# Kernel tuning notes

Hardware: AMD Instinct MI355X
Metric: run time of the kernel (lower is better)

Reference implementation:

```python
import jax, jax.numpy as jnp
import numpy as np

N, E = 50000, 800000
IN_C, HID, OUT_C, HEADS = 256, 32, 16, 8
NEG_SLOPE = 0.2


def gat_conv(x, edge_index, W, att_src, att_dst, bias, heads, out_c, concat):
    """PyG-style GATConv (inference, dropout off, add_self_loops=True).

    x: [N, F_in], edge_index: [2, E] with row0=src(j), row1=dst(i).
    W: [F_in, heads*out_c], att_src/att_dst: [heads, out_c], bias: [heads*out_c] or [out_c].
    """
    n = x.shape[0]
    loops = jnp.arange(n, dtype=edge_index.dtype)
    src = jnp.concatenate([edge_index[0], loops])
    dst = jnp.concatenate([edge_index[1], loops])

    xl = (x @ W).reshape(n, heads, out_c)              # [N, H, C]
    a_src = jnp.einsum('nhc,hc->nh', xl, att_src)      # [N, H]
    a_dst = jnp.einsum('nhc,hc->nh', xl, att_dst)

    e = a_src[src] + a_dst[dst]                        # [E', H]
    e = jnp.where(e >= 0, e, NEG_SLOPE * e)            # leaky_relu
    e_max = jax.ops.segment_max(e, dst, num_segments=n)
    e_exp = jnp.exp(e - e_max[dst])
    denom = jax.ops.segment_sum(e_exp, dst, num_segments=n)
    alpha = e_exp / (denom[dst] + 1e-16)               # segment softmax over in-edges of dst

    msg = alpha[:, :, None] * xl[src]                  # [E', H, C]
    out = jax.ops.segment_sum(msg, dst, num_segments=n)  # [N, H, C]
    if concat:
        out = out.reshape(n, heads * out_c)
    else:
        out = out.mean(axis=1)
    return out + bias


def setup_inputs() -> dict:
    key = jax.random.key(0)
    ks = jax.random.split(key, 10)
    s_in = 1.0 / np.sqrt(IN_C)
    s_h = 1.0 / np.sqrt(HEADS * HID)
    x = jax.random.normal(ks[0], (N, IN_C), dtype=jnp.float32)
    edge_index = jax.random.randint(ks[1], (2, E), 0, N, dtype=jnp.int64)
    return {
        'x': x,
        'edge_index': edge_index,
        'W1': jax.random.normal(ks[2], (IN_C, HEADS * HID), dtype=jnp.float32) * s_in,
        'att_src1': jax.random.normal(ks[3], (HEADS, HID), dtype=jnp.float32) * s_h,
        'att_dst1': jax.random.normal(ks[4], (HEADS, HID), dtype=jnp.float32) * s_h,
        'b1': jnp.zeros((HEADS * HID,), dtype=jnp.float32),
        'W2': jax.random.normal(ks[5], (HEADS * HID, OUT_C), dtype=jnp.float32) * s_h,
        'att_src2': jax.random.normal(ks[6], (1, OUT_C), dtype=jnp.float32) * 0.1,
        'att_dst2': jax.random.normal(ks[7], (1, OUT_C), dtype=jnp.float32) * 0.1,
        'b2': jnp.zeros((OUT_C,), dtype=jnp.float32),
    }


def reference(x, edge_index, W1, att_src1, att_dst1, b1, W2, att_src2, att_dst2, b2):
    h = gat_conv(x, edge_index, W1, att_src1, att_dst1, b1, HEADS, HID, concat=True)
    h = jax.nn.relu(h)
    # F.dropout(training=False) is identity at inference
    out = gat_conv(h, edge_index, W2, att_src2, att_dst2, b2, 1, OUT_C, concat=False)
    return jax.nn.log_softmax(out, axis=1)
```

## Files before the change

kernel.cpp:

```cpp
#include <hip/hip_runtime.h>

#define IN_C 256
#define H1 8
#define C1 32
#define F1 256
#define OC 16
#define NEG 0.2f

typedef short short8 __attribute__((ext_vector_type(8)));
typedef unsigned short ushort8 __attribute__((ext_vector_type(8)));
typedef float floatx4 __attribute__((ext_vector_type(4)));

__device__ __forceinline__ unsigned short f2bf(float f) {
    unsigned u = __builtin_bit_cast(unsigned, f);
    u = (u + 0x7fffu + ((u >> 16) & 1u)) >> 16;
    return (unsigned short)u;
}
__device__ __forceinline__ float bf2f(unsigned short h) {
    unsigned u = ((unsigned)h) << 16;
    return __builtin_bit_cast(float, u);
}

__global__ __launch_bounds__(256) void k_cvt_x(const float* __restrict__ x,
                                               unsigned short* __restrict__ xb, int n4)
{
    int idx = blockIdx.x * 256 + threadIdx.x;
    if (idx >= n4) return;
    float4 v = ((const float4*)x)[idx];
    ushort4 o;
    o.x = f2bf(v.x); o.y = f2bf(v.y); o.z = f2bf(v.z); o.w = f2bf(v.w);
    ((ushort4*)xb)[idx] = o;
}

__global__ __launch_bounds__(256) void k_wcvt(const float* __restrict__ W1,
                                              const float* __restrict__ W2,
                                              unsigned short* __restrict__ w1t,
                                              unsigned short* __restrict__ w2t)
{
    int idx = blockIdx.x * 256 + threadIdx.x;
    if (idx < 65536) {
        int n = idx >> 8, k = idx & 255;
        w1t[n * 256 + k] = f2bf(W1[k * 256 + n]);
    } else if (idx < 65536 + 4096) {
        int r = idx - 65536;
        int n = r >> 8, k = r & 255;
        w2t[n * 256 + k] = f2bf(W2[k * 16 + n]);
    }
}

__global__ __launch_bounds__(256) void k_gemm1(const unsigned short* __restrict__ A,
                                               const unsigned short* __restrict__ Bt,
                                               unsigned short* __restrict__ Cb, int M)
{
    __shared__ short As[128][40];
    __shared__ short Bs[128][40];
    const int tid  = threadIdx.x;
    const int lane = tid & 63;
    const int w    = tid >> 6;
    const int bm   = blockIdx.x * 128;
    const int bn   = blockIdx.y * 128;
    const int wm   = (w >> 1) * 64;
    const int wn   = (w & 1) * 64;
    const int srow = tid >> 1;
    const int soff = (tid & 1) * 16;
    floatx4 acc[4][4] = {};
    for (int k0 = 0; k0 < 256; k0 += 32) {
        __syncthreads();
        {
            int gr = bm + srow;
            ushort8 v0 = {0,0,0,0,0,0,0,0}, v1 = {0,0,0,0,0,0,0,0};
            if (gr < M) {
                const ushort8* p = (const ushort8*)(A + (size_t)gr * 256 + k0 + soff);
                v0 = p[0]; v1 = p[1];
            }
            *(ushort8*)&As[srow][soff]     = v0;
            *(ushort8*)&As[srow][soff + 8] = v1;
        }
        {
            const ushort8* p = (const ushort8*)(Bt + (size_t)(bn + srow) * 256 + k0 + soff);
            *(ushort8*)&Bs[srow][soff]     = p[0];
            *(ushort8*)&Bs[srow][soff + 8] = p[1];
        }
        __syncthreads();
        short8 af[4], bf[4];
        const int q8 = (lane >> 4) * 8;
        const int l15 = lane & 15;
#pragma unroll
        for (int i = 0; i < 4; ++i) af[i] = *(const short8*)&As[wm + i * 16 + l15][q8];
#pragma unroll
        for (int j = 0; j < 4; ++j) bf[j] = *(const short8*)&Bs[wn + j * 16 + l15][q8];
#pragma unroll
        for (int i = 0; i < 4; ++i)
#pragma unroll
            for (int j = 0; j < 4; ++j)
                acc[i][j] = __builtin_amdgcn_mfma_f32_16x16x32_bf16(af[i], bf[j], acc[i][j], 0, 0, 0);
    }
    const int l15 = lane & 15;
    const int rq  = (lane >> 4) * 4;
#pragma unroll
    for (int i = 0; i < 4; ++i) {
#pragma unroll
        for (int reg = 0; reg < 4; ++reg) {
            int gr = bm + wm + i * 16 + rq + reg;
            if (gr < M) {
#pragma unroll
                for (int j = 0; j < 4; ++j)
                    Cb[(size_t)gr * 256 + bn + wn + j * 16 + l15] = f2bf(acc[i][j][reg]);
            }
        }
    }
}

__global__ __launch_bounds__(256) void k_att1(const unsigned short* __restrict__ xl,
                                              const float* __restrict__ att_s,
                                              const float* __restrict__ att_d,
                                              float* __restrict__ asrc,
                                              float* __restrict__ adst, int N)
{
    int idx = blockIdx.x * 256 + threadIdx.x;
    if (idx >= N * H1) return;
    int i = idx >> 3, h = idx & 7;
    const ushort4* xr = (const ushort4*)(xl + (size_t)i * F1 + h * C1);
    const float* s = att_s + h * C1;
    const float* d = att_d + h * C1;
    float s1 = 0.f, s2 = 0.f;
#pragma unroll
    for (int c4 = 0; c4 < 8; ++c4) {
        ushort4 v = xr[c4];
        float f0 = bf2f(v.x), f1 = bf2f(v.y), f2 = bf2f(v.z), f3 = bf2f(v.w);
        int c = c4 * 4;
        s1 += f0 * s[c] + f1 * s[c+1] + f2 * s[c+2] + f3 * s[c+3];
        s2 += f0 * d[c] + f1 * d[c+1] + f2 * d[c+2] + f3 * d[c+3];
    }
    asrc[idx] = s1; adst[idx] = s2;
}

__global__ __launch_bounds__(256) void k_hist(const int* __restrict__ ei,
                                              int* __restrict__ cnt, int E)
{
    int e = blockIdx.x * 256 + threadIdx.x;
    if (e < E) atomicAdd(&cnt[ei[E + e]], 1);
}

__global__ __launch_bounds__(256) void k_scan_a(const int* __restrict__ cnt,
                                                int* __restrict__ rp,
                                                int* __restrict__ bsum, int N)
{
    __shared__ int ws4[4];
    int t = threadIdx.x, lane = t & 63, wid = t >> 6;
    int i = blockIdx.x * 256 + t;
    int v = (i < N) ? cnt[i] : 0;
    int incl = v;
#pragma unroll
    for (int off = 1; off < 64; off <<= 1) {
        int tv = __shfl_up(incl, off, 64);
        if (lane >= off) incl += tv;
    }
    if (lane == 63) ws4[wid] = incl;
    __syncthreads();
    int add = 0;
    for (int w = 0; w < wid; ++w) add += ws4[w];
    incl += add;
    if (i < N) rp[i + 1] = incl;
    if (t == 255) bsum[blockIdx.x] = incl;
}

__global__ __launch_bounds__(256) void k_scan_b(const int* __restrict__ bsum,
                                                int* __restrict__ boff, int NB)
{
    __shared__ int ws4[4];
    int t = threadIdx.x, lane = t & 63, wid = t >> 6;
    int i0 = t * 4;
    int v[4];
#pragma unroll
    for (int k = 0; k < 4; ++k) { int i = i0 + k; v[k] = (i < NB) ? bsum[i] : 0; }
    int s = v[0] + v[1] + v[2] + v[3];
    int incl = s;
#pragma unroll
    for (int off = 1; off < 64; off <<= 1) {
        int tv = __shfl_up(incl, off, 64);
        if (lane >= off) incl += tv;
    }
    if (lane == 63) ws4[wid] = incl;
    __syncthreads();
    int wpre = 0;
    for (int w = 0; w < wid; ++w) wpre += ws4[w];
    int run = wpre + incl - s;
#pragma unroll
    for (int k = 0; k < 4; ++k) {
        int i = i0 + k;
        if (i < NB) boff[i] = run;
        run += v[k];
    }
}

__global__ __launch_bounds__(256) void k_scan_c(int* __restrict__ rp,
                                                const int* __restrict__ boff, int N)
{
    int i = blockIdx.x * 256 + threadIdx.x;
    if (i < N) rp[i + 1] += boff[blockIdx.x];
    if (i == 0) rp[0] = 0;
}

__global__ __launch_bounds__(256) void k_scatter(const int* __restrict__ ei,
                                                 int* __restrict__ cur,
                                                 int* __restrict__ ssrc, int E)
{
    int e = blockIdx.x * 256 + threadIdx.x;
    if (e >= E) return;
    int s = ei[e];
    int d = ei[E + e];
    int pos = atomicAdd(&cur[d], 1);
    ssrc[pos] = s;
}

__global__ __launch_bounds__(256) void k_gather1(const int* __restrict__ rp,
                                                 const int* __restrict__ ssrc,
                                                 const unsigned short* __restrict__ xl,
                                                 const float* __restrict__ asrc,
                                                 const float* __restrict__ adst,
                                                 const float* __restrict__ bias,
                                                 unsigned short* __restrict__ hout, int N)
{
    int lane = threadIdx.x & 63;
    int node = blockIdx.x * 4 + (threadIdx.x >> 6);
    if (node >= N) return;
    int h  = lane >> 3;
    int cb = lane * 4;
    float ad = adst[(size_t)node * H1 + h];
    float e = asrc[(size_t)node * H1 + h] + ad;
    e = e >= 0.f ? e : NEG * e;
    float w = __expf(e);
    ushort4 xv = *(const ushort4*)(xl + (size_t)node * F1 + cb);
    float ax = w * bf2f(xv.x), ay = w * bf2f(xv.y), az = w * bf2f(xv.z), aw = w * bf2f(xv.w);
    float den = w;
    int jb = rp[node], je = rp[node + 1];
    int j = jb;
    for (; j + 4 <= je; j += 4) {
        int s0 = ssrc[j], s1 = ssrc[j+1], s2 = ssrc[j+2], s3 = ssrc[j+3];
        float e0 = asrc[(size_t)s0 * H1 + h] + ad;
        float e1 = asrc[(size_t)s1 * H1 + h] + ad;
        float e2 = asrc[(size_t)s2 * H1 + h] + ad;
        float e3 = asrc[(size_t)s3 * H1 + h] + ad;
        ushort4 r0 = *(const ushort4*)(xl + (size_t)s0 * F1 + cb);
        ushort4 r1 = *(const ushort4*)(xl + (size_t)s1 * F1 + cb);
        ushort4 r2 = *(const ushort4*)(xl + (size_t)s2 * F1 + cb);
        ushort4 r3 = *(const ushort4*)(xl + (size_t)s3 * F1 + cb);
        e0 = e0 >= 0.f ? e0 : NEG * e0;  float w0 = __expf(e0);
        e1 = e1 >= 0.f ? e1 : NEG * e1;  float w1 = __expf(e1);
        e2 = e2 >= 0.f ? e2 : NEG * e2;  float w2 = __expf(e2);
        e3 = e3 >= 0.f ? e3 : NEG * e3;  float w3 = __expf(e3);
        den += w0 + w1 + w2 + w3;
        ax += w0*bf2f(r0.x) + w1*bf2f(r1.x) + w2*bf2f(r2.x) + w3*bf2f(r3.x);
        ay += w0*bf2f(r0.y) + w1*bf2f(r1.y) + w2*bf2f(r2.y) + w3*bf2f(r3.y);
        az += w0*bf2f(r0.z) + w1*bf2f(r1.z) + w2*bf2f(r2.z) + w3*bf2f(r3.z);
        aw += w0*bf2f(r0.w) + w1*bf2f(r1.w) + w2*bf2f(r2.w) + w3*bf2f(r3.w);
    }
    for (; j < je; ++j) {
        int s = ssrc[j];
        float ev = asrc[(size_t)s * H1 + h] + ad;
        ev = ev >= 0.f ? ev : NEG * ev;
        float wv = __expf(ev);
        ushort4 sv = *(const ushort4*)(xl + (size_t)s * F1 + cb);
        ax += wv * bf2f(sv.x); ay += wv * bf2f(sv.y);
        az += wv * bf2f(sv.z); aw += wv * bf2f(sv.w);
        den += wv;
    }
    float inv = 1.f / (den + 1e-16f);
    float4 bv = *(const float4*)(bias + cb);
    ushort4 o;
    o.x = f2bf(fmaxf(ax * inv + bv.x, 0.f));
    o.y = f2bf(fmaxf(ay * inv + bv.y, 0.f));
    o.z = f2bf(fmaxf(az * inv + bv.z, 0.f));
    o.w = f2bf(fmaxf(aw * inv + bv.w, 0.f));
    *(ushort4*)(hout + (size_t)node * F1 + cb) = o;
}

__global__ __launch_bounds__(256) void k_gemm2(const unsigned short* __restrict__ Hm,
                                               const unsigned short* __restrict__ W2t,
                                               const float* __restrict__ as2,
                                               const float* __restrict__ ad2,
                                               unsigned short* __restrict__ xl2b,
                                               float* __restrict__ asrc,
                                               float* __restrict__ adst, int N)
{
    const int lane = threadIdx.x & 63;
    const int wid  = threadIdx.x >> 6;
    const int rowbase = blockIdx.x * 64 + wid * 16;
    const int col = lane & 15;
    const int q8  = (lane >> 4) * 8;
    const int m   = rowbase + col;
    const bool mv = m < N;
    const unsigned short* arow = Hm + (size_t)m * 256 + q8;
    const unsigned short* brow = W2t + (size_t)col * 256 + q8;
    floatx4 acc = {0.f, 0.f, 0.f, 0.f};
#pragma unroll
    for (int t = 0; t < 8; ++t) {
        short8 af = {0,0,0,0,0,0,0,0};
        if (mv) af = *(const short8*)(arow + t * 32);
        short8 bf = *(const short8*)(brow + t * 32);
        acc = __builtin_amdgcn_mfma_f32_16x16x32_bf16(af, bf, acc, 0, 0, 0);
    }
    float s_as = as2[col], s_ad = ad2[col];
    const int rq = (lane >> 4) * 4;
#pragma unroll
    for (int reg = 0; reg < 4; ++reg) {
        int row = rowbase + rq + reg;
        float v = acc[reg];
        float s1 = v * s_as, s2 = v * s_ad;
#pragma unroll
        for (int o = 1; o < 16; o <<= 1) { s1 += __shfl_xor(s1, o, 16); s2 += __shfl_xor(s2, o, 16); }
        if (row < N) {
            xl2b[(size_t)row * OC + col] = f2bf(v);
            if (col == 0) { asrc[row] = s1; adst[row] = s2; }
        }
    }
}

__global__ __launch_bounds__(256) void k_gather2(const int* __restrict__ rp,
                                                 const int* __restrict__ ssrc,
                                                 const unsigned short* __restrict__ xl2b,
                                                 const float* __restrict__ asrc,
                                                 const float* __restrict__ adst,
                                                 const float* __restrict__ bias,
                                                 float* __restrict__ out, int N)
{
    int sub  = threadIdx.x & 15;
    int node = blockIdx.x * 16 + (threadIdx.x >> 4);
    if (node >= N) return;
    float ad = adst[node];
    float e = asrc[node] + ad;
    e = e >= 0.f ? e : NEG * e;
    float w = __expf(e);
    float acc = w * bf2f(xl2b[(size_t)node * OC + sub]);
    float den = w;
    int jb = rp[node], je = rp[node + 1];
    int j = jb;
    for (; j + 4 <= je; j += 4) {
        int s0 = ssrc[j], s1i = ssrc[j+1], s2i = ssrc[j+2], s3i = ssrc[j+3];
        float e0 = asrc[s0] + ad, e1 = asrc[s1i] + ad, e2 = asrc[s2i] + ad, e3 = asrc[s3i] + ad;
        float v0 = bf2f(xl2b[(size_t)s0 * OC + sub]);
        float v1 = bf2f(xl2b[(size_t)s1i * OC + sub]);
        float v2 = bf2f(xl2b[(size_t)s2i * OC + sub]);
        float v3 = bf2f(xl2b[(size_t)s3i * OC + sub]);
        e0 = e0 >= 0.f ? e0 : NEG * e0;  float w0 = __expf(e0);
        e1 = e1 >= 0.f ? e1 : NEG * e1;  float w1 = __expf(e1);
        e2 = e2 >= 0.f ? e2 : NEG * e2;  float w2 = __expf(e2);
        e3 = e3 >= 0.f ? e3 : NEG * e3;  float w3 = __expf(e3);
        den += w0 + w1 + w2 + w3;
        acc += w0 * v0 + w1 * v1 + w2 * v2 + w3 * v3;
    }
    for (; j < je; ++j) {
        int s = ssrc[j];
        float ev = asrc[s] + ad;
        ev = ev >= 0.f ? ev : NEG * ev;
        float wv = __expf(ev);
        acc += wv * bf2f(xl2b[(size_t)s * OC + sub]);
        den += wv;
    }
    float v = acc / (den + 1e-16f) + bias[sub];
    float m = v;
#pragma unroll
    for (int o = 1; o < 16; o <<= 1) m = fmaxf(m, __shfl_xor(m, o, 16));
    float ex = __expf(v - m);
    float ss = ex;
#pragma unroll
    for (int o = 1; o < 16; o <<= 1) ss += __shfl_xor(ss, o, 16);
    out[(size_t)node * OC + sub] = v - m - logf(ss);
}

extern "C" void kernel_launch(void* const* d_in, const int* in_sizes, int n_in,
                              void* d_out, int out_size, void* d_ws, size_t ws_size,
                              hipStream_t stream)
{
    const float* x   = (const float*)d_in[0];
    const int*   ei  = (const int*)d_in[1];
    const float* W1  = (const float*)d_in[2];
    const float* as1 = (const float*)d_in[3];
    const float* ad1 = (const float*)d_in[4];
    const float* b1  = (const float*)d_in[5];
    const float* W2  = (const float*)d_in[6];
    const float* as2 = (const float*)d_in[7];
    const float* ad2 = (const float*)d_in[8];
    const float* b2  = (const float*)d_in[9];
    float* out = (float*)d_out;

    const int N = in_sizes[0] / IN_C;
    const int E = in_sizes[1] / 2;
    const int NB = (N + 255) / 256;

    char* base = (char*)d_ws;
    unsigned short* xb   = (unsigned short*)base;
    unsigned short* xl1b = xb + (size_t)N * F1;
    unsigned short* hb   = xl1b + (size_t)N * F1;
    unsigned short* w1t  = hb + (size_t)N * F1;
    unsigned short* w2t  = w1t + 256 * 256;
    unsigned short* xl2b = w2t + 16 * 256;
    float* asrc1 = (float*)(xl2b + (size_t)N * OC);
    float* adst1 = asrc1 + (size_t)N * H1;
    float* asrc2 = adst1 + (size_t)N * H1;
    float* adst2 = asrc2 + N;
    int*   rp    = (int*)(adst2 + N);
    int*   cnt   = rp + (N + 1);
    int*   cur   = cnt + N;
    int*   bsum  = cur + N;
    int*   boff  = bsum + 1024;
    int*   ssrc  = boff + 1024;

    hipMemsetAsync(cnt, 0, (size_t)N * sizeof(int), stream);
    k_hist<<<(E + 255) / 256, 256, 0, stream>>>(ei, cnt, E);
    k_scan_a<<<NB, 256, 0, stream>>>(cnt, rp, bsum, N);
    k_scan_b<<<1, 256, 0, stream>>>(bsum, boff, NB);
    k_scan_c<<<NB, 256, 0, stream>>>(rp, boff, N);
    hipMemcpyAsync(cur, rp, (size_t)N * sizeof(int), hipMemcpyDeviceToDevice, stream);
    k_scatter<<<(E + 255) / 256, 256, 0, stream>>>(ei, cur, ssrc, E);

    k_cvt_x<<<(N * 64 + 255) / 256, 256, 0, stream>>>(x, xb, N * 64);
    k_wcvt<<<(65536 + 4096) / 256, 256, 0, stream>>>(W1, W2, w1t, w2t);

    k_gemm1<<<dim3((N + 127) / 128, 2), 256, 0, stream>>>(xb, w1t, xl1b, N);
    k_att1<<<(N * H1 + 255) / 256, 256, 0, stream>>>(xl1b, as1, ad1, asrc1, adst1, N);
    k_gather1<<<(N + 3) / 4, 256, 0, stream>>>(rp, ssrc, xl1b, asrc1, adst1, b1, hb, N);

    k_gemm2<<<(N + 63) / 64, 256, 0, stream>>>(hb, w2t, as2, ad2, xl2b, asrc2, adst2, N);
    k_gather2<<<(N + 15) / 16, 256, 0, stream>>>(rp, ssrc, xl2b, asrc2, adst2, b2, out, N);
}
```

Measured before the change: 338.5 us.

## Split per-node edge aggregation across multiple waves/slots in both gather kernels

In the first-layer gather, each node's in-edge range is now split in half between two wavefronts, and the partial sums are combined through shared memory after a block barrier. In the second-layer gather, each node gets a full wavefront whose four 16-lane slots walk the edge list in stride 4, then reduce with cross-lane shuffles. Both aim to raise memory-level parallelism for these latency-bound random gathers. The cost is more threads per node, a block barrier in gather1, extra shuffle work in gather2, and the loss of the 4-way unroll in gather2.

```diff
diff --git a/kernel.cpp b/kernel.cpp
--- a/kernel.cpp
+++ b/kernel.cpp
@@ -222,58 +222,84 @@
                                                  const float* __restrict__ bias,
                                                  unsigned short* __restrict__ hout, int N)
 {
-    int lane = threadIdx.x & 63;
-    int node = blockIdx.x * 4 + (threadIdx.x >> 6);
-    if (node >= N) return;
+    __shared__ float accs[2][256];
+    __shared__ float dens[2][8];
+    int tid  = threadIdx.x;
+    int lane = tid & 63;
+    int pair = tid >> 7;
+    int half = (tid >> 6) & 1;
+    int node = blockIdx.x * 2 + pair;
+    bool valid = node < N;
     int h  = lane >> 3;
     int cb = lane * 4;
-    float ad = adst[(size_t)node * H1 + h];
-    float e = asrc[(size_t)node * H1 + h] + ad;
-    e = e >= 0.f ? e : NEG * e;
-    float w = __expf(e);
-    ushort4 xv = *(const ushort4*)(xl + (size_t)node * F1 + cb);
-    float ax = w * bf2f(xv.x), ay = w * bf2f(xv.y), az = w * bf2f(xv.z), aw = w * bf2f(xv.w);
-    float den = w;
-    int jb = rp[node], je = rp[node + 1];
-    int j = jb;
-    for (; j + 4 <= je; j += 4) {
-        int s0 = ssrc[j], s1 = ssrc[j+1], s2 = ssrc[j+2], s3 = ssrc[j+3];
-        float e0 = asrc[(size_t)s0 * H1 + h] + ad;
-        float e1 = asrc[(size_t)s1 * H1 + h] + ad;
-        float e2 = asrc[(size_t)s2 * H1 + h] + ad;
-        float e3 = asrc[(size_t)s3 * H1 + h] + ad;
-        ushort4 r0 = *(const ushort4*)(xl + (size_t)s0 * F1 + cb);
-        ushort4 r1 = *(const ushort4*)(xl + (size_t)s1 * F1 + cb);
-        ushort4 r2 = *(const ushort4*)(xl + (size_t)s2 * F1 + cb);
-        ushort4 r3 = *(const ushort4*)(xl + (size_t)s3 * F1 + cb);
-        e0 = e0 >= 0.f ? e0 : NEG * e0;  float w0 = __expf(e0);
-        e1 = e1 >= 0.f ? e1 : NEG * e1;  float w1 = __expf(e1);
-        e2 = e2 >= 0.f ? e2 : NEG * e2;  float w2 = __expf(e2);
-        e3 = e3 >= 0.f ? e3 : NEG * e3;  float w3 = __expf(e3);
-        den += w0 + w1 + w2 + w3;
-        ax += w0*bf2f(r0.x) + w1*bf2f(r1.x) + w2*bf2f(r2.x) + w3*bf2f(r3.x);
-        ay += w0*bf2f(r0.y) + w1*bf2f(r1.y) + w2*bf2f(r2.y) + w3*bf2f(r3.y);
-        az += w0*bf2f(r0.z) + w1*bf2f(r1.z) + w2*bf2f(r2.z) + w3*bf2f(r3.z);
-        aw += w0*bf2f(r0.w) + w1*bf2f(r1.w) + w2*bf2f(r2.w) + w3*bf2f(r3.w);
-    }
-    for (; j < je; ++j) {
-        int s = ssrc[j];
-        float ev = asrc[(size_t)s * H1 + h] + ad;
-        ev = ev >= 0.f ? ev : NEG * ev;
-        float wv = __expf(ev);
-        ushort4 sv = *(const ushort4*)(xl + (size_t)s * F1 + cb);
-        ax += wv * bf2f(sv.x); ay += wv * bf2f(sv.y);
-        az += wv * bf2f(sv.z); aw += wv * bf2f(sv.w);
-        den += wv;
-    }
-    float inv = 1.f / (den + 1e-16f);
-    float4 bv = *(const float4*)(bias + cb);
-    ushort4 o;
-    o.x = f2bf(fmaxf(ax * inv + bv.x, 0.f));
-    o.y = f2bf(fmaxf(ay * inv + bv.y, 0.f));
-    o.z = f2bf(fmaxf(az * inv + bv.z, 0.f));
-    o.w = f2bf(fmaxf(aw * inv + bv.w, 0.f));
-    *(ushort4*)(hout + (size_t)node * F1 + cb) = o;
+    float ax = 0.f, ay = 0.f, az = 0.f, aw = 0.f, den = 0.f;
+    float ad = 0.f;
+    if (valid) {
+        ad = adst[(size_t)node * H1 + h];
+        int jb0 = rp[node], je0 = rp[node + 1];
+        int mid = (jb0 + je0) >> 1;
+        int jb = half ? mid : jb0;
+        int je = half ? je0 : mid;
+        if (half == 0) {
+            float e = asrc[(size_t)node * H1 + h] + ad;
+            e = e >= 0.f ? e : NEG * e;
+            float w = __expf(e);
+            ushort4 xv = *(const ushort4*)(xl + (size_t)node * F1 + cb);
+            ax = w * bf2f(xv.x); ay = w * bf2f(xv.y);
+            az = w * bf2f(xv.z); aw = w * bf2f(xv.w);
+            den = w;
+        }
+        int j = jb;
+        for (; j + 4 <= je; j += 4) {
+            int s0 = ssrc[j], s1 = ssrc[j+1], s2 = ssrc[j+2], s3 = ssrc[j+3];
+            float e0 = asrc[(size_t)s0 * H1 + h] + ad;
+            float e1 = asrc[(size_t)s1 * H1 + h] + ad;
+            float e2 = asrc[(size_t)s2 * H1 + h] + ad;
+            float e3 = asrc[(size_t)s3 * H1 + h] + ad;
+            ushort4 r0 = *(const ushort4*)(xl + (size_t)s0 * F1 + cb);
+            ushort4 r1 = *(const ushort4*)(xl + (size_t)s1 * F1 + cb);
+            ushort4 r2 = *(const ushort4*)(xl + (size_t)s2 * F1 + cb);
+            ushort4 r3 = *(const ushort4*)(xl + (size_t)s3 * F1 + cb);
+            e0 = e0 >= 0.f ? e0 : NEG * e0;  float w0 = __expf(e0);
+            e1 = e1 >= 0.f ? e1 : NEG * e1;  float w1 = __expf(e1);
+            e2 = e2 >= 0.f ? e2 : NEG * e2;  float w2 = __expf(e2);
+            e3 = e3 >= 0.f ? e3 : NEG * e3;  float w3 = __expf(e3);
+            den += w0 + w1 + w2 + w3;
+            ax += w0*bf2f(r0.x) + w1*bf2f(r1.x) + w2*bf2f(r2.x) + w3*bf2f(r3.x);
+            ay += w0*bf2f(r0.y) + w1*bf2f(r1.y) + w2*bf2f(r2.y) + w3*bf2f(r3.y);
+            az += w0*bf2f(r0.z) + w1*bf2f(r1.z) + w2*bf2f(r2.z) + w3*bf2f(r3.z);
+            aw += w0*bf2f(r0.w) + w1*bf2f(r1.w) + w2*bf2f(r2.w) + w3*bf2f(r3.w);
+        }
+        for (; j < je; ++j) {
+            int s = ssrc[j];
+            float ev = asrc[(size_t)s * H1 + h] + ad;
+            ev = ev >= 0.f ? ev : NEG * ev;
+            float wv = __expf(ev);
+            ushort4 sv = *(const ushort4*)(xl + (size_t)s * F1 + cb);
+            ax += wv * bf2f(sv.x); ay += wv * bf2f(sv.y);
+            az += wv * bf2f(sv.z); aw += wv * bf2f(sv.w);
+            den += wv;
+        }
+    }
+    if (half == 1) {
+        accs[pair][cb+0] = ax; accs[pair][cb+1] = ay;
+        accs[pair][cb+2] = az; accs[pair][cb+3] = aw;
+        if ((lane & 7) == 0) dens[pair][h] = den;
+    }
+    __syncthreads();
+    if (half == 0 && valid) {
+        ax += accs[pair][cb+0]; ay += accs[pair][cb+1];
+        az += accs[pair][cb+2]; aw += accs[pair][cb+3];
+        den += dens[pair][h];
+        float inv = 1.f / (den + 1e-16f);
+        float4 bv = *(const float4*)(bias + cb);
+        ushort4 o;
+        o.x = f2bf(fmaxf(ax * inv + bv.x, 0.f));
+        o.y = f2bf(fmaxf(ay * inv + bv.y, 0.f));
+        o.z = f2bf(fmaxf(az * inv + bv.z, 0.f));
+        o.w = f2bf(fmaxf(aw * inv + bv.w, 0.f));
+        *(ushort4*)(hout + (size_t)node * F1 + cb) = o;
+    }
 }
 
 __global__ __launch_bounds__(256) void k_gemm2(const unsigned short* __restrict__ Hm,
@@ -325,32 +351,22 @@
                                                  const float* __restrict__ bias,
                                                  float* __restrict__ out, int N)
 {
-    int sub  = threadIdx.x & 15;
-    int node = blockIdx.x * 16 + (threadIdx.x >> 4);
+    int lane = threadIdx.x & 63;
+    int slot = lane >> 4;
+    int sub  = lane & 15;
+    int node = blockIdx.x * 4 + (threadIdx.x >> 6);
     if (node >= N) return;
     float ad = adst[node];
-    float e = asrc[node] + ad;
-    e = e >= 0.f ? e : NEG * e;
-    float w = __expf(e);
-    float acc = w * bf2f(xl2b[(size_t)node * OC + sub]);
-    float den = w;
+    float acc = 0.f, den = 0.f;
+    if (slot == 0) {
+        float e = asrc[node] + ad;
+        e = e >= 0.f ? e : NEG * e;
+        float w = __expf(e);
+        acc = w * bf2f(xl2b[(size_t)node * OC + sub]);
+        den = w;
+    }
     int jb = rp[node], je = rp[node + 1];
-    int j = jb;
-    for (; j + 4 <= je; j += 4) {
-        int s0 = ssrc[j], s1i = ssrc[j+1], s2i = ssrc[j+2], s3i = ssrc[j+3];
-        float e0 = asrc[s0] + ad, e1 = asrc[s1i] + ad, e2 = asrc[s2i] + ad, e3 = asrc[s3i] + ad;
-        float v0 = bf2f(xl2b[(size_t)s0 * OC + sub]);
-        float v1 = bf2f(xl2b[(size_t)s1i * OC + sub]);
-        float v2 = bf2f(xl2b[(size_t)s2i * OC + sub]);
-        float v3 = bf2f(xl2b[(size_t)s3i * OC + sub]);
-        e0 = e0 >= 0.f ? e0 : NEG * e0;  float w0 = __expf(e0);
-        e1 = e1 >= 0.f ? e1 : NEG * e1;  float w1 = __expf(e1);
-        e2 = e2 >= 0.f ? e2 : NEG * e2;  float w2 = __expf(e2);
-        e3 = e3 >= 0.f ? e3 : NEG * e3;  float w3 = __expf(e3);
-        den += w0 + w1 + w2 + w3;
-        acc += w0 * v0 + w1 * v1 + w2 * v2 + w3 * v3;
-    }
-    for (; j < je; ++j) {
+    for (int j = jb + slot; j < je; j += 4) {
         int s = ssrc[j];
         float ev = asrc[s] + ad;
         ev = ev >= 0.f ? ev : NEG * ev;
@@ -358,15 +374,19 @@
         acc += wv * bf2f(xl2b[(size_t)s * OC + sub]);
         den += wv;
     }
-    float v = acc / (den + 1e-16f) + bias[sub];
-    float m = v;
-#pragma unroll
-    for (int o = 1; o < 16; o <<= 1) m = fmaxf(m, __shfl_xor(m, o, 16));
-    float ex = __expf(v - m);
-    float ss = ex;
-#pragma unroll
-    for (int o = 1; o < 16; o <<= 1) ss += __shfl_xor(ss, o, 16);
-    out[(size_t)node * OC + sub] = v - m - logf(ss);
+    acc += __shfl_xor(acc, 16, 64);  den += __shfl_xor(den, 16, 64);
+    acc += __shfl_xor(acc, 32, 64);  den += __shfl_xor(den, 32, 64);
+    if (slot == 0) {
+        float v = acc / (den + 1e-16f) + bias[sub];
+        float m = v;
+#pragma unroll
+        for (int o = 1; o < 16; o <<= 1) m = fmaxf(m, __shfl_xor(m, o, 16));
+        float ex = __expf(v - m);
+        float ss = ex;
+#pragma unroll
+        for (int o = 1; o < 16; o <<= 1) ss += __shfl_xor(ss, o, 16);
+        out[(size_t)node * OC + sub] = v - m - logf(ss);
+    }
 }
 
 extern "C" void kernel_launch(void* const* d_in, const int* in_sizes, int n_in,
@@ -420,8 +440,8 @@
 
     k_gemm1<<<dim3((N + 127) / 128, 2), 256, 0, stream>>>(xb, w1t, xl1b, N);
     k_att1<<<(N * H1 + 255) / 256, 256, 0, stream>>>(xl1b, as1, ad1, asrc1, adst1, N);
-    k_gather1<<<(N + 3) / 4, 256, 0, stream>>>(rp, ssrc, xl1b, asrc1, adst1, b1, hb, N);
+    k_gather1<<<(N + 1) / 2, 256, 0, stream>>>(rp, ssrc, xl1b, asrc1, adst1, b1, hb, N);
 
     k_gemm2<<<(N + 63) / 64, 256, 0, stream>>>(hb, w2t, as2, ad2, xl2b, asrc2, adst2, N);
-    k_gather2<<<(N + 15) / 16, 256, 0, stream>>>(rp, ssrc, xl2b, asrc2, adst2, b2, out, N);
-}
+    k_gather2<<<(N + 3) / 4, 256, 0, stream>>>(rp, ssrc, xl2b, asrc2, adst2, b2, out, N);
+}
```

Result: slower. 356.7 us (+5.4%).

## Fuse x bf16 conversion into GEMM1 and merge small preprocessing kernels

Applied to the files above, without the earlier changes.

Removes the separate x-to-bf16 conversion pass: GEMM1 now loads fp32 rows directly and converts to bf16 while staging into shared memory. It also folds the weight transpose/convert into the histogram kernel and replaces the cur memcpy by computing cur inside the final scan kernel. This saves a full read and write of a bf16 copy of x plus several launches, at the cost of GEMM1 reading x as fp32 twice, once per N-block column.

```diff
diff --git a/kernel.cpp b/kernel.cpp
--- a/kernel.cpp
+++ b/kernel.cpp
@@ -21,34 +21,26 @@
     return __builtin_bit_cast(float, u);
 }
 
-__global__ __launch_bounds__(256) void k_cvt_x(const float* __restrict__ x,
-                                               unsigned short* __restrict__ xb, int n4)
-{
-    int idx = blockIdx.x * 256 + threadIdx.x;
-    if (idx >= n4) return;
-    float4 v = ((const float4*)x)[idx];
-    ushort4 o;
-    o.x = f2bf(v.x); o.y = f2bf(v.y); o.z = f2bf(v.z); o.w = f2bf(v.w);
-    ((ushort4*)xb)[idx] = o;
-}
-
-__global__ __launch_bounds__(256) void k_wcvt(const float* __restrict__ W1,
-                                              const float* __restrict__ W2,
-                                              unsigned short* __restrict__ w1t,
-                                              unsigned short* __restrict__ w2t)
-{
-    int idx = blockIdx.x * 256 + threadIdx.x;
-    if (idx < 65536) {
-        int n = idx >> 8, k = idx & 255;
+__global__ __launch_bounds__(256) void k_fuse0(const int* __restrict__ ei,
+                                               int* __restrict__ cnt,
+                                               const float* __restrict__ W1,
+                                               const float* __restrict__ W2,
+                                               unsigned short* __restrict__ w1t,
+                                               unsigned short* __restrict__ w2t, int E)
+{
+    int gid = blockIdx.x * 256 + threadIdx.x;
+    if (gid < E) atomicAdd(&cnt[ei[E + gid]], 1);
+    if (gid < 65536) {
+        int n = gid >> 8, k = gid & 255;
         w1t[n * 256 + k] = f2bf(W1[k * 256 + n]);
-    } else if (idx < 65536 + 4096) {
-        int r = idx - 65536;
+    } else if (gid < 65536 + 4096) {
+        int r = gid - 65536;
         int n = r >> 8, k = r & 255;
         w2t[n * 256 + k] = f2bf(W2[k * 16 + n]);
     }
 }
 
-__global__ __launch_bounds__(256) void k_gemm1(const unsigned short* __restrict__ A,
+__global__ __launch_bounds__(256) void k_gemm1(const float* __restrict__ A,
                                                const unsigned short* __restrict__ Bt,
                                                unsigned short* __restrict__ Cb, int M)
 {
@@ -68,11 +60,16 @@
         __syncthreads();
         {
             int gr = bm + srow;
-            ushort8 v0 = {0,0,0,0,0,0,0,0}, v1 = {0,0,0,0,0,0,0,0};
+            float4 f0 = {0,0,0,0}, f1 = {0,0,0,0}, f2 = {0,0,0,0}, f3 = {0,0,0,0};
             if (gr < M) {
-                const ushort8* p = (const ushort8*)(A + (size_t)gr * 256 + k0 + soff);
-                v0 = p[0]; v1 = p[1];
+                const float4* p = (const float4*)(A + (size_t)gr * 256 + k0 + soff);
+                f0 = p[0]; f1 = p[1]; f2 = p[2]; f3 = p[3];
             }
+            ushort8 v0, v1;
+            v0[0]=f2bf(f0.x); v0[1]=f2bf(f0.y); v0[2]=f2bf(f0.z); v0[3]=f2bf(f0.w);
+            v0[4]=f2bf(f1.x); v0[5]=f2bf(f1.y); v0[6]=f2bf(f1.z); v0[7]=f2bf(f1.w);
+            v1[0]=f2bf(f2.x); v1[1]=f2bf(f2.y); v1[2]=f2bf(f2.z); v1[3]=f2bf(f2.w);
+            v1[4]=f2bf(f3.x); v1[5]=f2bf(f3.y); v1[6]=f2bf(f3.z); v1[7]=f2bf(f3.w);
             *(ushort8*)&As[srow][soff]     = v0;
             *(ushort8*)&As[srow][soff + 8] = v1;
         }
@@ -135,13 +132,6 @@
     asrc[idx] = s1; adst[idx] = s2;
 }
 
-__global__ __launch_bounds__(256) void k_hist(const int* __restrict__ ei,
-                                              int* __restrict__ cnt, int E)
-{
-    int e = blockIdx.x * 256 + threadIdx.x;
-    if (e < E) atomicAdd(&cnt[ei[E + e]], 1);
-}
-
 __global__ __launch_bounds__(256) void k_scan_a(const int* __restrict__ cnt,
                                                 int* __restrict__ rp,
                                                 int* __restrict__ bsum, int N)
@@ -195,10 +185,16 @@
 }
 
 __global__ __launch_bounds__(256) void k_scan_c(int* __restrict__ rp,
-                                                const int* __restrict__ boff, int N)
+                                                const int* __restrict__ boff,
+                                                const int* __restrict__ cnt,
+                                                int* __restrict__ cur, int N)
 {
     int i = blockIdx.x * 256 + threadIdx.x;
-    if (i < N) rp[i + 1] += boff[blockIdx.x];
+    if (i < N) {
+        int v = rp[i + 1] + boff[blockIdx.x];
+        rp[i + 1] = v;
+        cur[i] = v - cnt[i];
+    }
     if (i == 0) rp[0] = 0;
 }
 
@@ -390,8 +386,7 @@
     const int NB = (N + 255) / 256;
 
     char* base = (char*)d_ws;
-    unsigned short* xb   = (unsigned short*)base;
-    unsigned short* xl1b = xb + (size_t)N * F1;
+    unsigned short* xl1b = (unsigned short*)base;
     unsigned short* hb   = xl1b + (size_t)N * F1;
     unsigned short* w1t  = hb + (size_t)N * F1;
     unsigned short* w2t  = w1t + 256 * 256;
@@ -408,17 +403,13 @@
     int*   ssrc  = boff + 1024;
 
     hipMemsetAsync(cnt, 0, (size_t)N * sizeof(int), stream);
-    k_hist<<<(E + 255) / 256, 256, 0, stream>>>(ei, cnt, E);
+    k_fuse0<<<(E + 255) / 256, 256, 0, stream>>>(ei, cnt, W1, W2, w1t, w2t, E);
     k_scan_a<<<NB, 256, 0, stream>>>(cnt, rp, bsum, N);
     k_scan_b<<<1, 256, 0, stream>>>(bsum, boff, NB);
-    k_scan_c<<<NB, 256, 0, stream>>>(rp, boff, N);
-    hipMemcpyAsync(cur, rp, (size_t)N * sizeof(int), hipMemcpyDeviceToDevice, stream);
+    k_scan_c<<<NB, 256, 0, stream>>>(rp, boff, cnt, cur, N);
     k_scatter<<<(E + 255) / 256, 256, 0, stream>>>(ei, cur, ssrc, E);
 
-    k_cvt_x<<<(N * 64 + 255) / 256, 256, 0, stream>>>(x, xb, N * 64);
-    k_wcvt<<<(65536 + 4096) / 256, 256, 0, stream>>>(W1, W2, w1t, w2t);
-
-    k_gemm1<<<dim3((N + 127) / 128, 2), 256, 0, stream>>>(xb, w1t, xl1b, N);
+    k_gemm1<<<dim3((N + 127) / 128, 2), 256, 0, stream>>>(x, w1t, xl1b, N);
     k_att1<<<(N * H1 + 255) / 256, 256, 0, stream>>>(xl1b, as1, ad1, asrc1, adst1, N);
     k_gather1<<<(N + 3) / 4, 256, 0, stream>>>(rp, ssrc, xl1b, asrc1, adst1, b1, hb, N);
 
```

Result: no change. 333.5 us (-1.5%).
